# Optimization experiments

Hardware: AMD Instinct MI355X
Metric: run time of the kernel (lower is better)

## Reference

```python
import jax, jax.numpy as jnp
import numpy as np

N_NODES = 50000
N_EDGES = 800000
IN_DIM = 64
HID = 64
OUT_DIM = 40
NEG_SLOPE = 0.2


def _gat_layer(x, src, dst, W, b, att, bias, n_nodes):
    # x: [N, Fin] -> lin -> [N, Fout]; heads = 1
    h = x @ W.T + b
    x_i = h[dst]                      # [E, F] target features
    x_j = h[src]                      # [E, F] source features
    # edge attention logits: cat([x_i, x_j]) @ att.T -> [E, 1]
    alpha = jnp.concatenate([x_i, x_j], axis=-1) @ att.T
    alpha = jax.nn.leaky_relu(alpha, NEG_SLOPE)
    # segment softmax over destination node (pyg_utils.softmax)
    amax = jax.ops.segment_max(alpha, dst, num_segments=n_nodes)
    e = jnp.exp(alpha - amax[dst])
    denom = jax.ops.segment_sum(e, dst, num_segments=n_nodes)
    alpha = e / (denom[dst] + 1e-16)
    # message = alpha * x_j, aggr='add' scatter to dst, then + bias
    out = jax.ops.segment_sum(x_j * alpha, dst, num_segments=n_nodes)
    return out + bias


def setup_inputs() -> dict:
    key = jax.random.key(0)
    ks = jax.random.split(key, 12)
    x = jax.random.normal(ks[0], (N_NODES, IN_DIM), dtype=jnp.float32)
    edge_index = jax.random.randint(ks[1], (2, N_EDGES), 0, N_NODES, dtype=jnp.int64)
    def glorot(k, shape):
        fan_in, fan_out = shape[1], shape[0]
        lim = float(np.sqrt(6.0 / (fan_in + fan_out)))
        return jax.random.uniform(k, shape, jnp.float32, -lim, lim)
    W1 = glorot(ks[2], (HID, IN_DIM))
    b1 = jnp.zeros((HID,), jnp.float32)
    att1 = glorot(ks[3], (1, 2 * HID))
    bias1 = jnp.zeros((HID,), jnp.float32)
    W2 = glorot(ks[4], (HID, HID))
    b2 = jnp.zeros((HID,), jnp.float32)
    att2 = glorot(ks[5], (1, 2 * HID))
    bias2 = jnp.zeros((HID,), jnp.float32)
    Wp1 = glorot(ks[6], (HID, HID))
    bp1 = jnp.zeros((HID,), jnp.float32)
    Wp2 = glorot(ks[7], (OUT_DIM, HID))
    bp2 = jnp.zeros((OUT_DIM,), jnp.float32)
    return {"x": x, "edge_index": edge_index,
            "W1": W1, "b1": b1, "att1": att1, "bias1": bias1,
            "W2": W2, "b2": b2, "att2": att2, "bias2": bias2,
            "Wp1": Wp1, "bp1": bp1, "Wp2": Wp2, "bp2": bp2}


def reference(x, edge_index, W1, b1, att1, bias1, W2, b2, att2, bias2,
              Wp1, bp1, Wp2, bp2):
    src, dst = edge_index[0], edge_index[1]
    n = x.shape[0]
    # layer 1 (GAT) + relu; dropout p=0 in eval -> identity
    h = jax.nn.relu(_gat_layer(x, src, dst, W1, b1, att1, bias1, n))
    # layer 2 (GAT) + relu
    h = jax.nn.relu(_gat_layer(h, src, dst, W2, b2, att2, bias2, n))
    # post-MP MLP + log_softmax over classes
    h = h @ Wp1.T + bp1
    logits = h @ Wp2.T + bp2
    return jax.nn.log_softmax(logits, axis=1)
```

## Files before the change

### kernel.cpp

```cpp
#include <hip/hip_runtime.h>
#include <hip/hip_fp16.h>
#include <math.h>

#define NN 50000
#define NE 800000
#define NEG 0.2f

#define NPB 128
#define CHK 6250
#define NBUK 98
#define LCAP 10240
#define GB 782

typedef __attribute__((ext_vector_type(8))) short short8v;
typedef __attribute__((ext_vector_type(4))) float f32x4;

__device__ __forceinline__ float lrelu(float x){ return x > 0.f ? x : NEG * x; }

__device__ __forceinline__ short bf16t(float x){ return (short)(__float_as_uint(x) >> 16); }
__device__ __forceinline__ float bf16tof(short s){
    return __uint_as_float(((unsigned)(unsigned short)s) << 16);
}

__device__ __forceinline__ void lin_body(int blk, int tid,
                                         const float* __restrict__ X,
                                         const float* __restrict__ W,
                                         const float* __restrict__ b,
                                         const float* __restrict__ att,
                                         __half* __restrict__ Hh,
                                         float* __restrict__ ad,
                                         float* __restrict__ as_, int n){
    int lane = tid & 63, wid = tid >> 6;
    int nb = blk * 64 + wid * 16;
    if (nb >= n) return;
    int r0 = lane & 15, rg = lane >> 4;

    short8v a_hi[2], a_lo[2];
    int arow = nb + r0; if (arow >= n) arow = n - 1;
    const float* xp = X + (size_t)arow * 64 + rg * 8;
    #pragma unroll
    for (int ks = 0; ks < 2; ++ks){
        #pragma unroll
        for (int j = 0; j < 8; ++j){
            float v = xp[ks * 32 + j];
            short h = bf16t(v);
            a_hi[ks][j] = h;
            a_lo[ks][j] = bf16t(v - bf16tof(h));
        }
    }

    f32x4 acc[4] = {{0,0,0,0},{0,0,0,0},{0,0,0,0},{0,0,0,0}};
    #pragma unroll
    for (int nt = 0; nt < 4; ++nt){
        const float* wp = W + (size_t)(nt * 16 + r0) * 64 + rg * 8;
        #pragma unroll
        for (int ks = 0; ks < 2; ++ks){
            short8v b_hi, b_lo;
            #pragma unroll
            for (int j = 0; j < 8; ++j){
                float v = wp[ks * 32 + j];
                short h = bf16t(v);
                b_hi[j] = h;
                b_lo[j] = bf16t(v - bf16tof(h));
            }
            acc[nt] = __builtin_amdgcn_mfma_f32_16x16x32_bf16(a_hi[ks], b_hi, acc[nt], 0, 0, 0);
            acc[nt] = __builtin_amdgcn_mfma_f32_16x16x32_bf16(a_hi[ks], b_lo, acc[nt], 0, 0, 0);
            acc[nt] = __builtin_amdgcn_mfma_f32_16x16x32_bf16(a_lo[ks], b_hi, acc[nt], 0, 0, 0);
        }
    }

    #pragma unroll
    for (int nt = 0; nt < 4; ++nt){
        float bb = b[nt * 16 + r0];
        #pragma unroll
        for (int q = 0; q < 4; ++q){
            int node = nb + rg * 4 + q;
            float v = acc[nt][q] + bb;
            acc[nt][q] = v;
            if (node < n) Hh[(size_t)node * 64 + nt * 16 + r0] = __float2half(v);
        }
    }

    float attd[4], atts[4];
    #pragma unroll
    for (int nt = 0; nt < 4; ++nt){
        attd[nt] = att[nt * 16 + r0];
        atts[nt] = att[64 + nt * 16 + r0];
    }
    #pragma unroll
    for (int q = 0; q < 4; ++q){
        float pd = 0.f, ps = 0.f;
        #pragma unroll
        for (int nt = 0; nt < 4; ++nt){
            pd = fmaf(attd[nt], acc[nt][q], pd);
            ps = fmaf(atts[nt], acc[nt][q], ps);
        }
        #pragma unroll
        for (int off = 8; off; off >>= 1){
            pd += __shfl_xor(pd, off);
            ps += __shfl_xor(ps, off);
        }
        int node = nb + rg * 4 + q;
        if (r0 == 0 && node < n){ ad[node] = pd; as_[node] = ps; }
    }
}

__global__ __launch_bounds__(256) void k_fuse0(const float* __restrict__ X,
                                               const float* __restrict__ W1,
                                               const float* __restrict__ b1,
                                               const float* __restrict__ att1,
                                               __half* __restrict__ Hh,
                                               float* __restrict__ ad,
                                               float* __restrict__ as_,
                                               const int* __restrict__ dst,
                                               int* __restrict__ counts,
                                               const float* __restrict__ Wp1,
                                               const float* __restrict__ bp1,
                                               const float* __restrict__ Wp2,
                                               const float* __restrict__ bp2,
                                               float* __restrict__ Wc,
                                               float* __restrict__ bc){
    __shared__ int c[NBUK];
    int tid = threadIdx.x, blk = blockIdx.x;
    if (blk < GB){
        lin_body(blk, tid, X, W1, b1, att1, Hh, ad, as_, NN);
    } else if (blk < GB + NPB){
        int cb = blk - GB;
        for (int i = tid; i < NBUK; i += 256) c[i] = 0;
        __syncthreads();
        int beg = cb * CHK, end = min(beg + CHK, NE);
        for (int i = beg + tid; i < end; i += 256) atomicAdd(&c[dst[i] >> 9], 1);
        __syncthreads();
        for (int i = tid; i < NBUK; i += 256) counts[i * NPB + cb] = c[i];
    } else {
        for (int idx = tid; idx < 2560; idx += 256){
            int cc = idx >> 6, k = idx & 63;
            float s = 0.f;
            #pragma unroll 8
            for (int j = 0; j < 64; ++j) s = fmaf(Wp2[cc * 64 + j], Wp1[j * 64 + k], s);
            Wc[idx] = s;
        }
        if (tid < 40){
            float s = bp2[tid];
            for (int j = 0; j < 64; ++j) s = fmaf(Wp2[tid * 64 + j], bp1[j], s);
            bc[tid] = s;
        }
    }
}

__global__ __launch_bounds__(NPB) void k_scan1(int* __restrict__ counts,
                                               int* __restrict__ tot){
    __shared__ int wsum[2];
    int b = blockIdx.x, tid = threadIdx.x, lane = tid & 63, wid = tid >> 6;
    int v = counts[b * NPB + tid];
    int incl = v;
    #pragma unroll
    for (int off = 1; off < 64; off <<= 1){
        int t = __shfl_up(incl, off);
        if (lane >= off) incl += t;
    }
    if (lane == 63) wsum[wid] = incl;
    __syncthreads();
    int excl = incl - v + (wid ? wsum[0] : 0);
    counts[b * NPB + tid] = excl;
    if (tid == NPB - 1) tot[b] = excl + v;
}

__device__ __forceinline__ void bbase_scan(const int* __restrict__ tot,
                                           int* bb, int* wsum, int tid){
    int lane = tid & 63, w2 = tid >> 6;
    int vv = 0, incl = 0;
    if (tid < 128){
        vv = (tid < NBUK) ? tot[tid] : 0;
        incl = vv;
        #pragma unroll
        for (int off = 1; off < 64; off <<= 1){
            int t = __shfl_up(incl, off);
            if (lane >= off) incl += t;
        }
        if (lane == 63) wsum[w2] = incl;
    }
    __syncthreads();
    if (tid < NBUK) bb[tid] = incl - vv + (w2 ? wsum[0] : 0);
    __syncthreads();
}

__global__ __launch_bounds__(256) void k_partC(const int* __restrict__ src,
                                               const int* __restrict__ dst,
                                               const int* __restrict__ cofs,
                                               const int* __restrict__ tot,
                                               unsigned* __restrict__ part){
    __shared__ int lcur[NBUK];
    __shared__ int bb[NBUK];
    __shared__ int wsum[2];
    int tid = threadIdx.x, blk = blockIdx.x;
    bbase_scan(tot, bb, wsum, tid);
    for (int i = tid; i < NBUK; i += 256) lcur[i] = bb[i] + cofs[i * NPB + blk];
    __syncthreads();
    int beg = blk * CHK, end = min(beg + CHK, NE);
    for (int i = beg + tid; i < end; i += 256){
        int d = dst[i];
        int pos = atomicAdd(&lcur[d >> 9], 1);
        part[pos] = ((unsigned)(d & 511) << 16) | (unsigned)src[i];
    }
}

__global__ __launch_bounds__(256) void k_buildD(const unsigned* __restrict__ part,
                                                const int* __restrict__ tot,
                                                int* __restrict__ rowstart,
                                                int* __restrict__ csr){
    __shared__ int hist[512], cur[512];
    __shared__ int csrbuf[LCAP];
    __shared__ int swave[4];
    __shared__ int bb[NBUK];
    __shared__ int wsum2[2];
    int tid = threadIdx.x, lane = tid & 63, wid = tid >> 6;
    int b = blockIdx.x;
    bbase_scan(tot, bb, wsum2, tid);
    int ebeg = bb[b], cnt = tot[b];

    for (int i = tid; i < 512; i += 256) hist[i] = 0;
    __syncthreads();
    for (int i = tid; i < cnt; i += 256) atomicAdd(&hist[part[ebeg + i] >> 16], 1);
    __syncthreads();

    int h0 = hist[2 * tid], h1 = hist[2 * tid + 1];
    int v = h0 + h1, incl = v;
    #pragma unroll
    for (int off = 1; off < 64; off <<= 1){
        int t = __shfl_up(incl, off);
        if (lane >= off) incl += t;
    }
    if (lane == 63) swave[wid] = incl;
    __syncthreads();
    int woff = 0;
    #pragma unroll
    for (int w = 0; w < 4; ++w) if (w < wid) woff += swave[w];
    int e0 = woff + incl - v;
    int e1 = e0 + h0;
    cur[2 * tid] = e0; cur[2 * tid + 1] = e1;
    int gi = b * 512 + 2 * tid;
    if (gi     <= NN) rowstart[gi]     = ebeg + e0;
    if (gi + 1 <= NN) rowstart[gi + 1] = ebeg + e1;
    __syncthreads();

    for (int i = tid; i < cnt; i += 256){
        unsigned u = part[ebeg + i];
        int lp = atomicAdd(&cur[u >> 16], 1);
        if (lp < LCAP) csrbuf[lp] = (int)(u & 0xFFFFu);
    }
    __syncthreads();
    int m = min(cnt, LCAP);
    for (int i = tid; i < m; i += 256) csr[ebeg + i] = csrbuf[i];
}

__global__ __launch_bounds__(256) void k_lin_mfma(const float* __restrict__ X,
                                                  const float* __restrict__ W,
                                                  const float* __restrict__ b,
                                                  const float* __restrict__ att,
                                                  __half* __restrict__ Hh,
                                                  float* __restrict__ ad,
                                                  float* __restrict__ as_, int n){
    lin_body(blockIdx.x, threadIdx.x, X, W, b, att, Hh, ad, as_, n);
}

__global__ __launch_bounds__(256) void k_agg(const __half2* __restrict__ H2,
                                             const float* __restrict__ ad,
                                             const float* __restrict__ as_,
                                             const int* __restrict__ rowstart,
                                             const int* __restrict__ csr,
                                             const float2* __restrict__ bias2,
                                             float2* __restrict__ OUT2, int n){
    __shared__ float e_sh[4][64];
    __shared__ int   s_sh[4][64];
    int tid = threadIdx.x, lane = tid & 63, wid = tid >> 6;
    int node = blockIdx.x * 4 + wid;
    if (node >= n) return;
    int beg = rowstart[node], end = rowstart[node + 1];
    float adn = ad[node];
    int half = lane >> 5, hl = lane & 31;

    float accx = 0.f, accy = 0.f, denom = 0.f;
    for (int cbeg = beg; cbeg < end; cbeg += 64){
        int k = cbeg + lane;
        bool valid = (k < end);
        int s = valid ? csr[k] : 0;
        float e = valid ? __expf(lrelu(adn + as_[s])) : 0.f;
        e_sh[wid][lane] = e;
        s_sh[wid][lane] = valid ? s : 0;
        float es = e;
        #pragma unroll
        for (int off = 32; off; off >>= 1) es += __shfl_xor(es, off);
        denom += es;
        int cnt = min(64, end - cbeg);
        for (int j = 0; j < cnt; j += 8){
            int i0 = j + half, i1 = j + 2 + half, i2 = j + 4 + half, i3 = j + 6 + half;
            int   s0 = s_sh[wid][i0], s1 = s_sh[wid][i1];
            int   s2 = s_sh[wid][i2], s3 = s_sh[wid][i3];
            float e0 = e_sh[wid][i0], e1 = e_sh[wid][i1];
            float e2 = e_sh[wid][i2], e3 = e_sh[wid][i3];
            float2 fa = __half22float2(H2[(size_t)s0 * 32 + hl]);
            float2 fb = __half22float2(H2[(size_t)s1 * 32 + hl]);
            float2 fc = __half22float2(H2[(size_t)s2 * 32 + hl]);
            float2 fd = __half22float2(H2[(size_t)s3 * 32 + hl]);
            accx = fmaf(e0, fa.x, accx); accy = fmaf(e0, fa.y, accy);
            accx = fmaf(e1, fb.x, accx); accy = fmaf(e1, fb.y, accy);
            accx = fmaf(e2, fc.x, accx); accy = fmaf(e2, fc.y, accy);
            accx = fmaf(e3, fd.x, accx); accy = fmaf(e3, fd.y, accy);
        }
    }
    accx += __shfl_xor(accx, 32);
    accy += __shfl_xor(accy, 32);
    if (half == 0){
        float2 bb = bias2[hl];
        float inv = 1.f / (denom + 1e-16f);
        float2 o;
        o.x = fmaxf(fmaf(accx, inv, bb.x), 0.f);
        o.y = fmaxf(fmaf(accy, inv, bb.y), 0.f);
        OUT2[(size_t)node * 32 + hl] = o;
    }
}

__global__ __launch_bounds__(256) void k_mlp_mfma(const float* __restrict__ G,
                                                  const float* __restrict__ Wc,
                                                  const float* __restrict__ bc,
                                                  float* __restrict__ out, int n){
    int lane = threadIdx.x & 63, wid = threadIdx.x >> 6;
    int nb = blockIdx.x * 64 + wid * 16;
    if (nb >= n) return;
    int r0 = lane & 15, rg = lane >> 4;

    short8v a_hi[2], a_lo[2];
    int arow = nb + r0; if (arow >= n) arow = n - 1;
    const float* gp = G + (size_t)arow * 64 + rg * 8;
    #pragma unroll
    for (int ks = 0; ks < 2; ++ks){
        #pragma unroll
        for (int j = 0; j < 8; ++j){
            float v = gp[ks * 32 + j];
            short h = bf16t(v);
            a_hi[ks][j] = h;
            a_lo[ks][j] = bf16t(v - bf16tof(h));
        }
    }

    f32x4 acc[3] = {{0,0,0,0},{0,0,0,0},{0,0,0,0}};
    #pragma unroll
    for (int nt = 0; nt < 3; ++nt){
        int f = nt * 16 + r0;
        int fr = (f < 40) ? f : 39;
        const float* wp = Wc + (size_t)fr * 64 + rg * 8;
        #pragma unroll
        for (int ks = 0; ks < 2; ++ks){
            short8v b_hi, b_lo;
            #pragma unroll
            for (int j = 0; j < 8; ++j){
                float v = wp[ks * 32 + j];
                short h = bf16t(v);
                b_hi[j] = h;
                b_lo[j] = bf16t(v - bf16tof(h));
            }
            acc[nt] = __builtin_amdgcn_mfma_f32_16x16x32_bf16(a_hi[ks], b_hi, acc[nt], 0, 0, 0);
            acc[nt] = __builtin_amdgcn_mfma_f32_16x16x32_bf16(a_hi[ks], b_lo, acc[nt], 0, 0, 0);
            acc[nt] = __builtin_amdgcn_mfma_f32_16x16x32_bf16(a_lo[ks], b_hi, acc[nt], 0, 0, 0);
        }
    }

    float bcv[3];
    #pragma unroll
    for (int nt = 0; nt < 3; ++nt){
        int f = nt * 16 + r0;
        bcv[nt] = (f < 40) ? bc[f] : 0.f;
    }

    #pragma unroll
    for (int q = 0; q < 4; ++q){
        int node = nb + rg * 4 + q;
        float l0 = acc[0][q] + bcv[0];
        float l1 = acc[1][q] + bcv[1];
        float l2 = (32 + r0 < 40) ? acc[2][q] + bcv[2] : -INFINITY;
        float m = fmaxf(l0, fmaxf(l1, l2));
        #pragma unroll
        for (int off = 8; off; off >>= 1) m = fmaxf(m, __shfl_xor(m, off));
        float s = __expf(l0 - m) + __expf(l1 - m) + ((32 + r0 < 40) ? __expf(l2 - m) : 0.f);
        #pragma unroll
        for (int off = 8; off; off >>= 1) s += __shfl_xor(s, off);
        float lse = m + __logf(s);
        if (node < n){
            out[(size_t)node * 40 + r0]      = l0 - lse;
            out[(size_t)node * 40 + 16 + r0] = l1 - lse;
            if (32 + r0 < 40) out[(size_t)node * 40 + 32 + r0] = l2 - lse;
        }
    }
}

extern "C" void kernel_launch(void* const* d_in, const int* in_sizes, int n_in,
                              void* d_out, int out_size, void* d_ws, size_t ws_size,
                              hipStream_t stream){
    const float* x     = (const float*)d_in[0];
    const int*   ei    = (const int*)  d_in[1];
    const float* W1    = (const float*)d_in[2];
    const float* b1    = (const float*)d_in[3];
    const float* att1  = (const float*)d_in[4];
    const float* bias1 = (const float*)d_in[5];
    const float* W2    = (const float*)d_in[6];
    const float* b2    = (const float*)d_in[7];
    const float* att2  = (const float*)d_in[8];
    const float* bias2 = (const float*)d_in[9];
    const float* Wp1   = (const float*)d_in[10];
    const float* bp1   = (const float*)d_in[11];
    const float* Wp2   = (const float*)d_in[12];
    const float* bp2   = (const float*)d_in[13];
    float* out = (float*)d_out;

    float*    base     = (float*)d_ws;
    float*    g        = base;
    __half*   hh       = (__half*)(base + 3200000);
    unsigned* part     = (unsigned*)(base + 4800000);
    int*      csr      = (int*)(base + 5600000);
    int*      counts   = (int*)(base + 6400000);
    int*      tot      = (int*)(base + 6412944);
    int*      rowstart = (int*)(base + 6413200);
    float*    ad       = base + 6463208;
    float*    as_      = base + 6513208;
    float*    Wc       = base + 6563208;
    float*    bc       = base + 6565768;

    const int* srcv = ei;
    const int* dstv = ei + NE;

    k_fuse0 <<<GB + NPB + 1, 256, 0, stream>>>(x, W1, b1, att1, hh, ad, as_,
                                               dstv, counts,
                                               Wp1, bp1, Wp2, bp2, Wc, bc);
    k_scan1 <<<NBUK, NPB, 0, stream>>>(counts, tot);
    k_partC <<<NPB, 256, 0, stream>>>(srcv, dstv, counts, tot, part);
    k_buildD<<<NBUK, 256, 0, stream>>>(part, tot, rowstart, csr);

    int nb = (NN + 3) / 4;
    k_agg     <<<nb, 256, 0, stream>>>((const __half2*)hh, ad, as_, rowstart, csr,
                                       (const float2*)bias1, (float2*)g, NN);
    k_lin_mfma<<<GB, 256, 0, stream>>>(g, W2, b2, att2, hh, ad, as_, NN);
    k_agg     <<<nb, 256, 0, stream>>>((const __half2*)hh, ad, as_, rowstart, csr,
                                       (const float2*)bias2, (float2*)g, NN);
    k_mlp_mfma<<<GB, 256, 0, stream>>>(g, Wc, bc, out, NN);
}
```

Measured before the change: 142.1 us.

## Fuse GAT aggregation with the following linear layer and with the MLP head

The per-node aggregation kernel is merged into the next stage. Each wave now aggregates a tile of 16 consecutive destination nodes into LDS, then runs the MFMA linear or MLP on that tile directly. This removes the fp32 intermediate feature buffer round trip through global memory and two kernel launches. The CSR now packs the local destination index next to the source, so the attention logits can be computed per edge in a flat chunked loop over the tile. The risks are fewer parallel waves, with each wave walking 16 nodes in sequence, and masked wasted lanes at node boundaries.

```diff
diff --git a/kernel.cpp b/kernel.cpp
--- a/kernel.cpp
+++ b/kernel.cpp
@@ -208,9 +208,9 @@
 __global__ __launch_bounds__(256) void k_buildD(const unsigned* __restrict__ part,
                                                 const int* __restrict__ tot,
                                                 int* __restrict__ rowstart,
-                                                int* __restrict__ csr){
+                                                unsigned* __restrict__ csr){
     __shared__ int hist[512], cur[512];
-    __shared__ int csrbuf[LCAP];
+    __shared__ unsigned csrbuf[LCAP];
     __shared__ int swave[4];
     __shared__ int bb[NBUK];
     __shared__ int wsum2[2];
@@ -247,109 +247,117 @@
     for (int i = tid; i < cnt; i += 256){
         unsigned u = part[ebeg + i];
         int lp = atomicAdd(&cur[u >> 16], 1);
-        if (lp < LCAP) csrbuf[lp] = (int)(u & 0xFFFFu);
+        if (lp < LCAP) csrbuf[lp] = u;
     }
     __syncthreads();
     int m = min(cnt, LCAP);
     for (int i = tid; i < m; i += 256) csr[ebeg + i] = csrbuf[i];
 }
 
-__global__ __launch_bounds__(256) void k_lin_mfma(const float* __restrict__ X,
-                                                  const float* __restrict__ W,
-                                                  const float* __restrict__ b,
-                                                  const float* __restrict__ att,
-                                                  __half* __restrict__ Hh,
-                                                  float* __restrict__ ad,
-                                                  float* __restrict__ as_, int n){
-    lin_body(blockIdx.x, threadIdx.x, X, W, b, att, Hh, ad, as_, n);
-}
-
-__global__ __launch_bounds__(256) void k_agg(const __half2* __restrict__ H2,
-                                             const float* __restrict__ ad,
-                                             const float* __restrict__ as_,
-                                             const int* __restrict__ rowstart,
-                                             const int* __restrict__ csr,
-                                             const float2* __restrict__ bias2,
-                                             float2* __restrict__ OUT2, int n){
+__device__ __forceinline__ void agg_tile(const __half2* __restrict__ H2,
+                                         const float* __restrict__ ad,
+                                         const float* __restrict__ as_,
+                                         const int* __restrict__ rowstart,
+                                         const unsigned* __restrict__ csr,
+                                         const float2* __restrict__ bias2,
+                                         float (*e_sh)[64], unsigned (*s_sh)[64],
+                                         float* gtw, int nb, int lane, int wid){
+    int half = lane >> 5, hl = lane & 31;
+    int bknode = nb & ~511;
+    int ebeg = rowstart[nb], eend = rowstart[nb + 16];
+    float2 bb = bias2[hl];
+
+    float accx = 0.f, accy = 0.f, den = 0.f;
+    int nrel = 0;
+    int bn = ebeg, en = rowstart[nb + 1];
+
+    for (int cb = ebeg; cb < eend && nrel < 16; cb += 64){
+        int k = cb + lane;
+        bool valid = k < eend;
+        unsigned u = valid ? csr[k] : 0u;
+        int s = (int)(u & 0xFFFFu);
+        int nd = bknode + (int)(u >> 16);
+        float e = valid ? __expf(lrelu(ad[nd] + as_[s])) : 0.f;
+        e_sh[wid][lane] = e;
+        s_sh[wid][lane] = (unsigned)s;
+        int chunk_hi = min(cb + 64, eend);
+        while (true){
+            int hi = min(en, chunk_hi);
+            int lo = max(bn, cb);
+            for (int j = lo; j < hi; j += 16){
+                #pragma unroll
+                for (int t = 0; t < 8; ++t){
+                    int it = j + 2 * t + half;
+                    int tt = min(it - cb, 63);
+                    float ee = e_sh[wid][tt];
+                    int ss = (int)s_sh[wid][tt];
+                    ee = (it < hi) ? ee : 0.f;
+                    float2 f = __half22float2(H2[(size_t)ss * 32 + hl]);
+                    accx = fmaf(ee, f.x, accx);
+                    accy = fmaf(ee, f.y, accy);
+                    den += ee;
+                }
+            }
+            if (en <= chunk_hi){
+                accx += __shfl_xor(accx, 32);
+                accy += __shfl_xor(accy, 32);
+                den  += __shfl_xor(den,  32);
+                float inv = 1.f / (den + 1e-16f);
+                gtw[nrel * 68 + 2 * hl]     = fmaxf(fmaf(accx, inv, bb.x), 0.f);
+                gtw[nrel * 68 + 2 * hl + 1] = fmaxf(fmaf(accy, inv, bb.y), 0.f);
+                accx = 0.f; accy = 0.f; den = 0.f;
+                ++nrel;
+                if (nrel == 16) break;
+                bn = en; en = rowstart[nb + nrel + 1];
+            } else break;
+        }
+    }
+    while (nrel < 16){
+        gtw[nrel * 68 + 2 * hl]     = fmaxf(bb.x, 0.f);
+        gtw[nrel * 68 + 2 * hl + 1] = fmaxf(bb.y, 0.f);
+        ++nrel;
+        if (nrel < 16){ bn = en; en = rowstart[nb + nrel + 1]; }
+    }
+}
+
+__global__ __launch_bounds__(256) void k_agglin(const __half2* __restrict__ H2,
+                                                const float* __restrict__ ad,
+                                                const float* __restrict__ as_,
+                                                const int* __restrict__ rowstart,
+                                                const unsigned* __restrict__ csr,
+                                                const float2* __restrict__ bias2,
+                                                const float* __restrict__ W,
+                                                const float* __restrict__ b,
+                                                const float* __restrict__ att,
+                                                __half* __restrict__ Hh,
+                                                float* __restrict__ ad_o,
+                                                float* __restrict__ as_o, int n){
     __shared__ float e_sh[4][64];
-    __shared__ int   s_sh[4][64];
+    __shared__ unsigned s_sh[4][64];
+    __shared__ float gt[4][16 * 68];
     int tid = threadIdx.x, lane = tid & 63, wid = tid >> 6;
-    int node = blockIdx.x * 4 + wid;
-    if (node >= n) return;
-    int beg = rowstart[node], end = rowstart[node + 1];
-    float adn = ad[node];
-    int half = lane >> 5, hl = lane & 31;
-
-    float accx = 0.f, accy = 0.f, denom = 0.f;
-    for (int cbeg = beg; cbeg < end; cbeg += 64){
-        int k = cbeg + lane;
-        bool valid = (k < end);
-        int s = valid ? csr[k] : 0;
-        float e = valid ? __expf(lrelu(adn + as_[s])) : 0.f;
-        e_sh[wid][lane] = e;
-        s_sh[wid][lane] = valid ? s : 0;
-        float es = e;
-        #pragma unroll
-        for (int off = 32; off; off >>= 1) es += __shfl_xor(es, off);
-        denom += es;
-        int cnt = min(64, end - cbeg);
-        for (int j = 0; j < cnt; j += 8){
-            int i0 = j + half, i1 = j + 2 + half, i2 = j + 4 + half, i3 = j + 6 + half;
-            int   s0 = s_sh[wid][i0], s1 = s_sh[wid][i1];
-            int   s2 = s_sh[wid][i2], s3 = s_sh[wid][i3];
-            float e0 = e_sh[wid][i0], e1 = e_sh[wid][i1];
-            float e2 = e_sh[wid][i2], e3 = e_sh[wid][i3];
-            float2 fa = __half22float2(H2[(size_t)s0 * 32 + hl]);
-            float2 fb = __half22float2(H2[(size_t)s1 * 32 + hl]);
-            float2 fc = __half22float2(H2[(size_t)s2 * 32 + hl]);
-            float2 fd = __half22float2(H2[(size_t)s3 * 32 + hl]);
-            accx = fmaf(e0, fa.x, accx); accy = fmaf(e0, fa.y, accy);
-            accx = fmaf(e1, fb.x, accx); accy = fmaf(e1, fb.y, accy);
-            accx = fmaf(e2, fc.x, accx); accy = fmaf(e2, fc.y, accy);
-            accx = fmaf(e3, fd.x, accx); accy = fmaf(e3, fd.y, accy);
-        }
-    }
-    accx += __shfl_xor(accx, 32);
-    accy += __shfl_xor(accy, 32);
-    if (half == 0){
-        float2 bb = bias2[hl];
-        float inv = 1.f / (denom + 1e-16f);
-        float2 o;
-        o.x = fmaxf(fmaf(accx, inv, bb.x), 0.f);
-        o.y = fmaxf(fmaf(accy, inv, bb.y), 0.f);
-        OUT2[(size_t)node * 32 + hl] = o;
-    }
-}
-
-__global__ __launch_bounds__(256) void k_mlp_mfma(const float* __restrict__ G,
-                                                  const float* __restrict__ Wc,
-                                                  const float* __restrict__ bc,
-                                                  float* __restrict__ out, int n){
-    int lane = threadIdx.x & 63, wid = threadIdx.x >> 6;
     int nb = blockIdx.x * 64 + wid * 16;
     if (nb >= n) return;
+
+    agg_tile(H2, ad, as_, rowstart, csr, bias2, e_sh, s_sh, gt[wid], nb, lane, wid);
+
     int r0 = lane & 15, rg = lane >> 4;
-
     short8v a_hi[2], a_lo[2];
-    int arow = nb + r0; if (arow >= n) arow = n - 1;
-    const float* gp = G + (size_t)arow * 64 + rg * 8;
     #pragma unroll
     for (int ks = 0; ks < 2; ++ks){
         #pragma unroll
         for (int j = 0; j < 8; ++j){
-            float v = gp[ks * 32 + j];
+            float v = gt[wid][r0 * 68 + ks * 32 + rg * 8 + j];
             short h = bf16t(v);
             a_hi[ks][j] = h;
             a_lo[ks][j] = bf16t(v - bf16tof(h));
         }
     }
 
-    f32x4 acc[3] = {{0,0,0,0},{0,0,0,0},{0,0,0,0}};
-    #pragma unroll
-    for (int nt = 0; nt < 3; ++nt){
-        int f = nt * 16 + r0;
-        int fr = (f < 40) ? f : 39;
-        const float* wp = Wc + (size_t)fr * 64 + rg * 8;
+    f32x4 acc[4] = {{0,0,0,0},{0,0,0,0},{0,0,0,0},{0,0,0,0}};
+    #pragma unroll
+    for (int nt = 0; nt < 4; ++nt){
+        const float* wp = W + (size_t)(nt * 16 + r0) * 64 + rg * 8;
         #pragma unroll
         for (int ks = 0; ks < 2; ++ks){
             short8v b_hi, b_lo;
@@ -366,6 +374,95 @@
         }
     }
 
+    #pragma unroll
+    for (int nt = 0; nt < 4; ++nt){
+        float bbv = b[nt * 16 + r0];
+        #pragma unroll
+        for (int q = 0; q < 4; ++q){
+            int node = nb + rg * 4 + q;
+            float v = acc[nt][q] + bbv;
+            acc[nt][q] = v;
+            Hh[(size_t)node * 64 + nt * 16 + r0] = __float2half(v);
+        }
+    }
+
+    float attd[4], atts[4];
+    #pragma unroll
+    for (int nt = 0; nt < 4; ++nt){
+        attd[nt] = att[nt * 16 + r0];
+        atts[nt] = att[64 + nt * 16 + r0];
+    }
+    #pragma unroll
+    for (int q = 0; q < 4; ++q){
+        float pd = 0.f, ps = 0.f;
+        #pragma unroll
+        for (int nt = 0; nt < 4; ++nt){
+            pd = fmaf(attd[nt], acc[nt][q], pd);
+            ps = fmaf(atts[nt], acc[nt][q], ps);
+        }
+        #pragma unroll
+        for (int off = 8; off; off >>= 1){
+            pd += __shfl_xor(pd, off);
+            ps += __shfl_xor(ps, off);
+        }
+        int node = nb + rg * 4 + q;
+        if (r0 == 0){ ad_o[node] = pd; as_o[node] = ps; }
+    }
+}
+
+__global__ __launch_bounds__(256) void k_aggmlp(const __half2* __restrict__ H2,
+                                                const float* __restrict__ ad,
+                                                const float* __restrict__ as_,
+                                                const int* __restrict__ rowstart,
+                                                const unsigned* __restrict__ csr,
+                                                const float2* __restrict__ bias2,
+                                                const float* __restrict__ Wc,
+                                                const float* __restrict__ bc,
+                                                float* __restrict__ out, int n){
+    __shared__ float e_sh[4][64];
+    __shared__ unsigned s_sh[4][64];
+    __shared__ float gt[4][16 * 68];
+    int tid = threadIdx.x, lane = tid & 63, wid = tid >> 6;
+    int nb = blockIdx.x * 64 + wid * 16;
+    if (nb >= n) return;
+
+    agg_tile(H2, ad, as_, rowstart, csr, bias2, e_sh, s_sh, gt[wid], nb, lane, wid);
+
+    int r0 = lane & 15, rg = lane >> 4;
+    short8v a_hi[2], a_lo[2];
+    #pragma unroll
+    for (int ks = 0; ks < 2; ++ks){
+        #pragma unroll
+        for (int j = 0; j < 8; ++j){
+            float v = gt[wid][r0 * 68 + ks * 32 + rg * 8 + j];
+            short h = bf16t(v);
+            a_hi[ks][j] = h;
+            a_lo[ks][j] = bf16t(v - bf16tof(h));
+        }
+    }
+
+    f32x4 acc[3] = {{0,0,0,0},{0,0,0,0},{0,0,0,0}};
+    #pragma unroll
+    for (int nt = 0; nt < 3; ++nt){
+        int f = nt * 16 + r0;
+        int fr = (f < 40) ? f : 39;
+        const float* wp = Wc + (size_t)fr * 64 + rg * 8;
+        #pragma unroll
+        for (int ks = 0; ks < 2; ++ks){
+            short8v b_hi, b_lo;
+            #pragma unroll
+            for (int j = 0; j < 8; ++j){
+                float v = wp[ks * 32 + j];
+                short h = bf16t(v);
+                b_hi[j] = h;
+                b_lo[j] = bf16t(v - bf16tof(h));
+            }
+            acc[nt] = __builtin_amdgcn_mfma_f32_16x16x32_bf16(a_hi[ks], b_hi, acc[nt], 0, 0, 0);
+            acc[nt] = __builtin_amdgcn_mfma_f32_16x16x32_bf16(a_hi[ks], b_lo, acc[nt], 0, 0, 0);
+            acc[nt] = __builtin_amdgcn_mfma_f32_16x16x32_bf16(a_lo[ks], b_hi, acc[nt], 0, 0, 0);
+        }
+    }
+
     float bcv[3];
     #pragma unroll
     for (int nt = 0; nt < 3; ++nt){
@@ -386,11 +483,9 @@
         #pragma unroll
         for (int off = 8; off; off >>= 1) s += __shfl_xor(s, off);
         float lse = m + __logf(s);
-        if (node < n){
-            out[(size_t)node * 40 + r0]      = l0 - lse;
-            out[(size_t)node * 40 + 16 + r0] = l1 - lse;
-            if (32 + r0 < 40) out[(size_t)node * 40 + 32 + r0] = l2 - lse;
-        }
+        out[(size_t)node * 40 + r0]      = l0 - lse;
+        out[(size_t)node * 40 + 16 + r0] = l1 - lse;
+        if (32 + r0 < 40) out[(size_t)node * 40 + 32 + r0] = l2 - lse;
     }
 }
 
@@ -414,33 +509,33 @@
     float* out = (float*)d_out;
 
     float*    base     = (float*)d_ws;
-    float*    g        = base;
-    __half*   hh       = (__half*)(base + 3200000);
-    unsigned* part     = (unsigned*)(base + 4800000);
-    int*      csr      = (int*)(base + 5600000);
-    int*      counts   = (int*)(base + 6400000);
-    int*      tot      = (int*)(base + 6412944);
-    int*      rowstart = (int*)(base + 6413200);
-    float*    ad       = base + 6463208;
-    float*    as_      = base + 6513208;
-    float*    Wc       = base + 6563208;
-    float*    bc       = base + 6565768;
+    __half*   hhA      = (__half*)base;
+    __half*   hhB      = (__half*)(base + 1600000);
+    unsigned* part     = (unsigned*)(base + 3200000);
+    unsigned* csr      = (unsigned*)(base + 4000000);
+    int*      counts   = (int*)(base + 4800000);
+    int*      tot      = (int*)(base + 4812944);
+    int*      rowstart = (int*)(base + 4813072);
+    float*    adA      = base + 4863080;
+    float*    asA      = base + 4913080;
+    float*    adB      = base + 4963080;
+    float*    asB      = base + 5013080;
+    float*    Wc       = base + 5063080;
+    float*    bc       = base + 5065640;
 
     const int* srcv = ei;
     const int* dstv = ei + NE;
 
-    k_fuse0 <<<GB + NPB + 1, 256, 0, stream>>>(x, W1, b1, att1, hh, ad, as_,
+    k_fuse0 <<<GB + NPB + 1, 256, 0, stream>>>(x, W1, b1, att1, hhA, adA, asA,
                                                dstv, counts,
                                                Wp1, bp1, Wp2, bp2, Wc, bc);
     k_scan1 <<<NBUK, NPB, 0, stream>>>(counts, tot);
     k_partC <<<NPB, 256, 0, stream>>>(srcv, dstv, counts, tot, part);
     k_buildD<<<NBUK, 256, 0, stream>>>(part, tot, rowstart, csr);
 
-    int nb = (NN + 3) / 4;
-    k_agg     <<<nb, 256, 0, stream>>>((const __half2*)hh, ad, as_, rowstart, csr,
-                                       (const float2*)bias1, (float2*)g, NN);
-    k_lin_mfma<<<GB, 256, 0, stream>>>(g, W2, b2, att2, hh, ad, as_, NN);
-    k_agg     <<<nb, 256, 0, stream>>>((const __half2*)hh, ad, as_, rowstart, csr,
-                                       (const float2*)bias2, (float2*)g, NN);
-    k_mlp_mfma<<<GB, 256, 0, stream>>>(g, Wc, bc, out, NN);
-}
+    k_agglin<<<GB, 256, 0, stream>>>((const __half2*)hhA, adA, asA, rowstart, csr,
+                                     (const float2*)bias1, W2, b2, att2,
+                                     hhB, adB, asB, NN);
+    k_aggmlp<<<GB, 256, 0, stream>>>((const __half2*)hhB, adB, asB, rowstart, csr,
+                                     (const float2*)bias2, Wc, bc, out, NN);
+}
```

Measured after the change: 146.9 us. +3.3%, slower.

## Fold bucket scan into partition and build kernels; deepen gather unroll

Applied to the files above, without the earlier changes.

Removes the separate k_scan1 launch. k_partC and k_buildD now recompute per-bucket totals and per-chunk prefixes straight from the raw count matrix, with each of the first 98 threads serially reading 128 counts. This trades one kernel launch and its dependency for redundant serial reads in every block. Separately, the aggregation inner loop now issues 8 independent half2 gathers per step instead of 4, exposing more memory-level parallelism at the cost of more registers. When an inner step runs past the valid edge count it reads stale shared-memory entries, but those should carry zero weight.

```diff
diff --git a/kernel.cpp b/kernel.cpp
--- a/kernel.cpp
+++ b/kernel.cpp
@@ -148,26 +148,7 @@
     }
 }
 
-__global__ __launch_bounds__(NPB) void k_scan1(int* __restrict__ counts,
-                                               int* __restrict__ tot){
-    __shared__ int wsum[2];
-    int b = blockIdx.x, tid = threadIdx.x, lane = tid & 63, wid = tid >> 6;
-    int v = counts[b * NPB + tid];
-    int incl = v;
-    #pragma unroll
-    for (int off = 1; off < 64; off <<= 1){
-        int t = __shfl_up(incl, off);
-        if (lane >= off) incl += t;
-    }
-    if (lane == 63) wsum[wid] = incl;
-    __syncthreads();
-    int excl = incl - v + (wid ? wsum[0] : 0);
-    counts[b * NPB + tid] = excl;
-    if (tid == NPB - 1) tot[b] = excl + v;
-}
-
-__device__ __forceinline__ void bbase_scan(const int* __restrict__ tot,
-                                           int* bb, int* wsum, int tid){
+__device__ __forceinline__ void bbase_scan(const int* tot, int* bb, int* wsum, int tid){
     int lane = tid & 63, w2 = tid >> 6;
     int vv = 0, incl = 0;
     if (tid < 128){
@@ -187,15 +168,27 @@
 
 __global__ __launch_bounds__(256) void k_partC(const int* __restrict__ src,
                                                const int* __restrict__ dst,
-                                               const int* __restrict__ cofs,
-                                               const int* __restrict__ tot,
+                                               const int* __restrict__ counts,
                                                unsigned* __restrict__ part){
     __shared__ int lcur[NBUK];
+    __shared__ int totsh[NBUK];
     __shared__ int bb[NBUK];
     __shared__ int wsum[2];
     int tid = threadIdx.x, blk = blockIdx.x;
-    bbase_scan(tot, bb, wsum, tid);
-    for (int i = tid; i < NBUK; i += 256) lcur[i] = bb[i] + cofs[i * NPB + blk];
+    if (tid < NBUK){
+        const int* row = counts + tid * NPB;
+        int pre = 0, tt = 0;
+        for (int i = 0; i < NPB; ++i){
+            int cc = row[i];
+            tt += cc;
+            pre += (i < blk) ? cc : 0;
+        }
+        totsh[tid] = tt;
+        lcur[tid] = pre;
+    }
+    __syncthreads();
+    bbase_scan(totsh, bb, wsum, tid);
+    if (tid < NBUK) lcur[tid] += bb[tid];
     __syncthreads();
     int beg = blk * CHK, end = min(beg + CHK, NE);
     for (int i = beg + tid; i < end; i += 256){
@@ -206,18 +199,26 @@
 }
 
 __global__ __launch_bounds__(256) void k_buildD(const unsigned* __restrict__ part,
-                                                const int* __restrict__ tot,
+                                                const int* __restrict__ counts,
                                                 int* __restrict__ rowstart,
                                                 int* __restrict__ csr){
     __shared__ int hist[512], cur[512];
     __shared__ int csrbuf[LCAP];
     __shared__ int swave[4];
+    __shared__ int totsh[NBUK];
     __shared__ int bb[NBUK];
     __shared__ int wsum2[2];
     int tid = threadIdx.x, lane = tid & 63, wid = tid >> 6;
     int b = blockIdx.x;
-    bbase_scan(tot, bb, wsum2, tid);
-    int ebeg = bb[b], cnt = tot[b];
+    if (tid < NBUK){
+        const int* row = counts + tid * NPB;
+        int tt = 0;
+        for (int i = 0; i < NPB; ++i) tt += row[i];
+        totsh[tid] = tt;
+    }
+    __syncthreads();
+    bbase_scan(totsh, bb, wsum2, tid);
+    int ebeg = bb[b], cnt = totsh[b];
 
     for (int i = tid; i < 512; i += 256) hist[i] = 0;
     __syncthreads();
@@ -293,20 +294,20 @@
         for (int off = 32; off; off >>= 1) es += __shfl_xor(es, off);
         denom += es;
         int cnt = min(64, end - cbeg);
-        for (int j = 0; j < cnt; j += 8){
-            int i0 = j + half, i1 = j + 2 + half, i2 = j + 4 + half, i3 = j + 6 + half;
-            int   s0 = s_sh[wid][i0], s1 = s_sh[wid][i1];
-            int   s2 = s_sh[wid][i2], s3 = s_sh[wid][i3];
-            float e0 = e_sh[wid][i0], e1 = e_sh[wid][i1];
-            float e2 = e_sh[wid][i2], e3 = e_sh[wid][i3];
-            float2 fa = __half22float2(H2[(size_t)s0 * 32 + hl]);
-            float2 fb = __half22float2(H2[(size_t)s1 * 32 + hl]);
-            float2 fc = __half22float2(H2[(size_t)s2 * 32 + hl]);
-            float2 fd = __half22float2(H2[(size_t)s3 * 32 + hl]);
-            accx = fmaf(e0, fa.x, accx); accy = fmaf(e0, fa.y, accy);
-            accx = fmaf(e1, fb.x, accx); accy = fmaf(e1, fb.y, accy);
-            accx = fmaf(e2, fc.x, accx); accy = fmaf(e2, fc.y, accy);
-            accx = fmaf(e3, fd.x, accx); accy = fmaf(e3, fd.y, accy);
+        for (int j = 0; j < cnt; j += 16){
+            float2 f[8]; float ee[8];
+            #pragma unroll
+            for (int t = 0; t < 8; ++t){
+                int idx = j + 2 * t + half;
+                int ss = s_sh[wid][idx];
+                ee[t] = e_sh[wid][idx];
+                f[t] = __half22float2(H2[(size_t)ss * 32 + hl]);
+            }
+            #pragma unroll
+            for (int t = 0; t < 8; ++t){
+                accx = fmaf(ee[t], f[t].x, accx);
+                accy = fmaf(ee[t], f[t].y, accy);
+            }
         }
     }
     accx += __shfl_xor(accx, 32);
@@ -419,7 +420,6 @@
     unsigned* part     = (unsigned*)(base + 4800000);
     int*      csr      = (int*)(base + 5600000);
     int*      counts   = (int*)(base + 6400000);
-    int*      tot      = (int*)(base + 6412944);
     int*      rowstart = (int*)(base + 6413200);
     float*    ad       = base + 6463208;
     float*    as_      = base + 6513208;
@@ -432,9 +432,8 @@
     k_fuse0 <<<GB + NPB + 1, 256, 0, stream>>>(x, W1, b1, att1, hh, ad, as_,
                                                dstv, counts,
                                                Wp1, bp1, Wp2, bp2, Wc, bc);
-    k_scan1 <<<NBUK, NPB, 0, stream>>>(counts, tot);
-    k_partC <<<NPB, 256, 0, stream>>>(srcv, dstv, counts, tot, part);
-    k_buildD<<<NBUK, 256, 0, stream>>>(part, tot, rowstart, csr);
+    k_partC <<<NPB, 256, 0, stream>>>(srcv, dstv, counts, part);
+    k_buildD<<<NBUK, 256, 0, stream>>>(part, counts, rowstart, csr);
 
     int nb = (NN + 3) / 4;
     k_agg     <<<nb, 256, 0, stream>>>((const __half2*)hh, ad, as_, rowstart, csr,
```

Measured after the change: 140.8 us. Within noise of the previous version (-0.9%).
